# Optimization experiments

Hardware: AMD Instinct MI355X
Metric: run time of the kernel (lower is better)

Reference implementation:

```python
import jax, jax.numpy as jnp
import numpy as np

D = 32          # graph size -> E = D*D independent tiny MLPs
E = D * D       # 1024 experts
BATCH = 1024    # number of time points
H = 64          # hidden width hard-coded in TApproximator


def setup_inputs() -> dict:
    key = jax.random.key(0)
    ks = jax.random.split(key, 10)
    T = jax.random.uniform(ks[0], (BATCH,), dtype=jnp.float32)
    # per-expert uniform noise k ~ U[0,1) of shape [E, BATCH, H] (torch.rand(x.shape) per layer)
    noise = jax.random.uniform(ks[1], (E, BATCH, H), dtype=jnp.float32)
    # fc1: Linear(1, 64, bias=False) per expert -> weight [E, H]
    W1 = jax.random.normal(ks[2], (E, H), dtype=jnp.float32)
    # fc2: Linear(64, 64) per expert
    W2 = jax.random.normal(ks[3], (E, H, H), dtype=jnp.float32) / jnp.sqrt(jnp.float32(H))
    b2 = jax.random.normal(ks[4], (E, H), dtype=jnp.float32) * 0.01
    # fc3: Linear(64, 1) per expert
    W3 = jax.random.normal(ks[5], (E, H), dtype=jnp.float32) / jnp.sqrt(jnp.float32(H))
    b3 = jax.random.normal(ks[6], (E,), dtype=jnp.float32) * 0.01
    alpha = jnp.array([0.1], dtype=jnp.float32)
    beta = jnp.array([100.0], dtype=jnp.float32)
    bias = jnp.array([1.0], dtype=jnp.float32)
    return {"T": T, "noise": noise, "W1": W1, "W2": W2, "b2": b2,
            "W3": W3, "b3": b3, "alpha": alpha, "beta": beta, "bias": bias}


def reference(T, noise, W1, W2, b2, W3, b3, alpha, beta, bias):
    # --- TApproximator, batched over E = d^2 experts ---
    # fc1(T): [E, BATCH, H]
    x1 = jnp.einsum('b,eh->ebh', T, W1)
    # b = k*4 - 2 - x ; x += b  ==> fc1 output exactly cancels (as in source)
    x = x1 + (noise * 4.0 - 2.0 - x1)
    h = jax.nn.sigmoid(x)
    # sigmoid(fc2(h)): batched [E,BATCH,H] @ [E,H,H]
    h2 = jax.nn.sigmoid(jnp.einsum('ebh,eho->ebo', h, W2) + b2[:, None, :])
    # fc3 -> scalar per expert: [E, BATCH]
    out = jnp.einsum('ebh,eh->eb', h2, W3) + b3[:, None]
    B_mat = out.T  # torch.cat(B, dim=1) -> [BATCH, E]
    # T_embed = 1/alpha * cos(beta*T + bias)
    T_embed = (1.0 / alpha[0]) * jnp.cos(beta[0] * T + bias[0])
    return B_mat, T_embed
```

## Files before the change

kernel.cpp:

```cpp
#include <hip/hip_runtime.h>
#include <math.h>

#define NE 1024
#define NB 1024
#define NH 64

typedef __attribute__((ext_vector_type(4))) float f32x4;
typedef __attribute__((ext_vector_type(8))) __bf16 bf16x8;
typedef __attribute__((ext_vector_type(8))) unsigned short u16x8;

__device__ __forceinline__ unsigned short f2bf_bits(float f) {
  unsigned int u = __float_as_uint(f);
  u += 0x7fffu + ((u >> 16) & 1u);
  return (unsigned short)(u >> 16);
}

__device__ __forceinline__ float fast_sigmoid(float x) {
  float e = __builtin_amdgcn_exp2f(x * -1.4426950408889634f);
  return __builtin_amdgcn_rcpf(1.0f + e);
}

__global__ __launch_bounds__(256, 4) void expert_kernel(
    const float* __restrict__ noise,
    const float* __restrict__ W2,
    const float* __restrict__ b2,
    const float* __restrict__ W3,
    const float* __restrict__ b3,
    float* __restrict__ out)
{
  const int e    = blockIdx.x;
  const int tid  = threadIdx.x;
  const int lane = tid & 63;
  const int wid  = tid >> 6;
  const int c    = lane & 15;
  const int quad = lane >> 4;

  __shared__ float lds_w2[NH * NH];

  const float* w2e = W2 + (size_t)e * NH * NH;
  #pragma unroll
  for (int i = 0; i < 4; ++i) {
    int idx = tid + i * 256;
    ((f32x4*)lds_w2)[idx] = ((const f32x4*)w2e)[idx];
  }
  __syncthreads();

  bf16x8 bfrag[2][4];
  #pragma unroll
  for (int kh = 0; kh < 2; ++kh) {
    #pragma unroll
    for (int nt = 0; nt < 4; ++nt) {
      u16x8 tmp;
      #pragma unroll
      for (int j = 0; j < 8; ++j) {
        float w = lds_w2[(kh * 32 + quad * 8 + j) * NH + nt * 16 + c];
        tmp[j] = f2bf_bits(w);
      }
      bfrag[kh][nt] = __builtin_bit_cast(bf16x8, tmp);
    }
  }

  float b2v[4], w3v[4];
  #pragma unroll
  for (int nt = 0; nt < 4; ++nt) {
    b2v[nt] = b2[e * NH + nt * 16 + c];
    w3v[nt] = W3[e * NH + nt * 16 + c];
  }
  const float b3v = b3[e];

  const float* nbase = noise + (size_t)e * NB * NH;
  const f32x4 vzero = {0.f, 0.f, 0.f, 0.f};

  for (int pass = 0; pass < NB / 64; ++pass) {
    const int row0 = pass * 64 + wid * 16;
    const float* rowp = nbase + (row0 + c) * NH;

    f32x4 k0 = *((const f32x4*)(rowp + quad * 8));
    f32x4 k1 = *((const f32x4*)(rowp + quad * 8 + 4));
    f32x4 k2 = *((const f32x4*)(rowp + 32 + quad * 8));
    f32x4 k3 = *((const f32x4*)(rowp + 32 + quad * 8 + 4));

    u16x8 a0u, a1u;
    #pragma unroll
    for (int j = 0; j < 4; ++j) {
      a0u[j]     = f2bf_bits(fast_sigmoid(4.0f * k0[j] - 2.0f));
      a0u[j + 4] = f2bf_bits(fast_sigmoid(4.0f * k1[j] - 2.0f));
      a1u[j]     = f2bf_bits(fast_sigmoid(4.0f * k2[j] - 2.0f));
      a1u[j + 4] = f2bf_bits(fast_sigmoid(4.0f * k3[j] - 2.0f));
    }
    bf16x8 a0 = __builtin_bit_cast(bf16x8, a0u);
    bf16x8 a1 = __builtin_bit_cast(bf16x8, a1u);

    f32x4 acc[4];
    #pragma unroll
    for (int nt = 0; nt < 4; ++nt) acc[nt] = vzero;
    #pragma unroll
    for (int nt = 0; nt < 4; ++nt) {
      acc[nt] = __builtin_amdgcn_mfma_f32_16x16x32_bf16(a0, bfrag[0][nt], acc[nt], 0, 0, 0);
      acc[nt] = __builtin_amdgcn_mfma_f32_16x16x32_bf16(a1, bfrag[1][nt], acc[nt], 0, 0, 0);
    }

    float partial[4] = {0.f, 0.f, 0.f, 0.f};
    #pragma unroll
    for (int nt = 0; nt < 4; ++nt) {
      #pragma unroll
      for (int r = 0; r < 4; ++r) {
        float h2 = fast_sigmoid(acc[nt][r] + b2v[nt]);
        partial[r] += h2 * w3v[nt];
      }
    }

    #pragma unroll
    for (int r = 0; r < 4; ++r) {
      float v = partial[r];
      v += __shfl_xor(v, 1, 64);
      v += __shfl_xor(v, 2, 64);
      v += __shfl_xor(v, 4, 64);
      v += __shfl_xor(v, 8, 64);
      partial[r] = v;
    }

    if (c == 0) {
      #pragma unroll
      for (int r = 0; r < 4; ++r) {
        int b = row0 + quad * 4 + r;
        out[(size_t)b * NE + e] = partial[r] + b3v;
      }
    }
  }
}

__global__ void tembed_kernel(const float* __restrict__ T,
                              const float* __restrict__ alpha,
                              const float* __restrict__ beta,
                              const float* __restrict__ bias,
                              float* __restrict__ out2) {
  int i = blockIdx.x * blockDim.x + threadIdx.x;
  if (i < NB) {
    out2[i] = (1.0f / alpha[0]) * cosf(beta[0] * T[i] + bias[0]);
  }
}

extern "C" void kernel_launch(void* const* d_in, const int* in_sizes, int n_in,
                              void* d_out, int out_size, void* d_ws, size_t ws_size,
                              hipStream_t stream) {
  const float* T     = (const float*)d_in[0];
  const float* noise = (const float*)d_in[1];
  const float* W2    = (const float*)d_in[3];
  const float* b2    = (const float*)d_in[4];
  const float* W3    = (const float*)d_in[5];
  const float* b3    = (const float*)d_in[6];
  const float* alpha = (const float*)d_in[7];
  const float* beta  = (const float*)d_in[8];
  const float* bias  = (const float*)d_in[9];
  float* out = (float*)d_out;

  hipLaunchKernelGGL(expert_kernel, dim3(NE), dim3(256), 0, stream,
                     noise, W2, b2, W3, b3, out);
  hipLaunchKernelGGL(tembed_kernel, dim3(NB / 256), dim3(256), 0, stream,
                     T, alpha, beta, bias, out + (size_t)NE * NB);
}
```

Baseline: 399.2 us.

## Replace sigmoids with polynomial approximations, cheaper bf16 packing, and prefetch noise

Both sigmoids are replaced by odd minimax polynomials. The second one clamps its input to [-4,4], so outputs for larger pre-activations are approximated. The bf16 conversion now uses round-half-up plus a byte-permute to pack two values per instruction. Noise rows for the next pass are loaded a pass ahead so the global-memory latency overlaps the current MFMA and epilogue work. The goal is to cut transcendental and ALU cost in a kernel that is largely memory-bound, at the cost of accuracy from the approximate sigmoid and the clamp.

```diff
diff --git a/kernel.cpp b/kernel.cpp
--- a/kernel.cpp
+++ b/kernel.cpp
@@ -7,17 +7,29 @@
 
 typedef __attribute__((ext_vector_type(4))) float f32x4;
 typedef __attribute__((ext_vector_type(8))) __bf16 bf16x8;
-typedef __attribute__((ext_vector_type(8))) unsigned short u16x8;
+typedef __attribute__((ext_vector_type(4))) unsigned int u32x4;
 
-__device__ __forceinline__ unsigned short f2bf_bits(float f) {
-  unsigned int u = __float_as_uint(f);
-  u += 0x7fffu + ((u >> 16) & 1u);
-  return (unsigned short)(u >> 16);
+__device__ __forceinline__ unsigned int pack_bf16(float f0, float f1) {
+  unsigned int u0 = __float_as_uint(f0) + 0x8000u;
+  unsigned int u1 = __float_as_uint(f1) + 0x8000u;
+  return __builtin_amdgcn_perm(u1, u0, 0x07060302u);
 }
 
-__device__ __forceinline__ float fast_sigmoid(float x) {
-  float e = __builtin_amdgcn_exp2f(x * -1.4426950408889634f);
-  return __builtin_amdgcn_rcpf(1.0f + e);
+__device__ __forceinline__ float sig_h(float k) {
+  float t  = __builtin_fmaf(4.0f, k, -2.0f);
+  float x2 = t * t;
+  float u  = __builtin_fmaf(x2, 1.24902e-3f, -1.98468e-2f);
+  u        = __builtin_fmaf(x2, u, 0.2498016f);
+  return __builtin_fmaf(t, u, 0.5f);
+}
+
+__device__ __forceinline__ float sig_2(float x) {
+  x        = __builtin_amdgcn_fmed3f(x, -4.0f, 4.0f);
+  float x2 = x * x;
+  float u  = __builtin_fmaf(x2, -2.81297e-5f, 1.11341e-3f);
+  u        = __builtin_fmaf(x2, u, -1.86412e-2f);
+  u        = __builtin_fmaf(x2, u, 0.2489492f);
+  return __builtin_fmaf(x, u, 0.5f);
 }
 
 __global__ __launch_bounds__(256, 4) void expert_kernel(
@@ -50,11 +62,12 @@
   for (int kh = 0; kh < 2; ++kh) {
     #pragma unroll
     for (int nt = 0; nt < 4; ++nt) {
-      u16x8 tmp;
+      u32x4 tmp;
       #pragma unroll
-      for (int j = 0; j < 8; ++j) {
-        float w = lds_w2[(kh * 32 + quad * 8 + j) * NH + nt * 16 + c];
-        tmp[j] = f2bf_bits(w);
+      for (int j = 0; j < 4; ++j) {
+        float w0 = lds_w2[(kh * 32 + quad * 8 + 2 * j)     * NH + nt * 16 + c];
+        float w1 = lds_w2[(kh * 32 + quad * 8 + 2 * j + 1) * NH + nt * 16 + c];
+        tmp[j] = pack_bf16(w0, w1);
       }
       bfrag[kh][nt] = __builtin_bit_cast(bf16x8, tmp);
     }
@@ -71,22 +84,28 @@
   const float* nbase = noise + (size_t)e * NB * NH;
   const f32x4 vzero = {0.f, 0.f, 0.f, 0.f};
 
+  const float* rowp = nbase + (wid * 16 + c) * NH;
+  f32x4 k0 = *((const f32x4*)(rowp + quad * 8));
+  f32x4 k1 = *((const f32x4*)(rowp + quad * 8 + 4));
+  f32x4 k2 = *((const f32x4*)(rowp + 32 + quad * 8));
+  f32x4 k3 = *((const f32x4*)(rowp + 32 + quad * 8 + 4));
+
+  #pragma unroll 1
   for (int pass = 0; pass < NB / 64; ++pass) {
-    const int row0 = pass * 64 + wid * 16;
-    const float* rowp = nbase + (row0 + c) * NH;
+    int np = pass + 1 < NB / 64 ? pass + 1 : NB / 64 - 1;
+    const float* nrowp = nbase + (np * 64 + wid * 16 + c) * NH;
+    f32x4 n0 = *((const f32x4*)(nrowp + quad * 8));
+    f32x4 n1 = *((const f32x4*)(nrowp + quad * 8 + 4));
+    f32x4 n2 = *((const f32x4*)(nrowp + 32 + quad * 8));
+    f32x4 n3 = *((const f32x4*)(nrowp + 32 + quad * 8 + 4));
 
-    f32x4 k0 = *((const f32x4*)(rowp + quad * 8));
-    f32x4 k1 = *((const f32x4*)(rowp + quad * 8 + 4));
-    f32x4 k2 = *((const f32x4*)(rowp + 32 + quad * 8));
-    f32x4 k3 = *((const f32x4*)(rowp + 32 + quad * 8 + 4));
-
-    u16x8 a0u, a1u;
+    u32x4 a0u, a1u;
     #pragma unroll
-    for (int j = 0; j < 4; ++j) {
-      a0u[j]     = f2bf_bits(fast_sigmoid(4.0f * k0[j] - 2.0f));
-      a0u[j + 4] = f2bf_bits(fast_sigmoid(4.0f * k1[j] - 2.0f));
-      a1u[j]     = f2bf_bits(fast_sigmoid(4.0f * k2[j] - 2.0f));
-      a1u[j + 4] = f2bf_bits(fast_sigmoid(4.0f * k3[j] - 2.0f));
+    for (int j = 0; j < 2; ++j) {
+      a0u[j]     = pack_bf16(sig_h(k0[2 * j]), sig_h(k0[2 * j + 1]));
+      a0u[j + 2] = pack_bf16(sig_h(k1[2 * j]), sig_h(k1[2 * j + 1]));
+      a1u[j]     = pack_bf16(sig_h(k2[2 * j]), sig_h(k2[2 * j + 1]));
+      a1u[j + 2] = pack_bf16(sig_h(k3[2 * j]), sig_h(k3[2 * j + 1]));
     }
     bf16x8 a0 = __builtin_bit_cast(bf16x8, a0u);
     bf16x8 a1 = __builtin_bit_cast(bf16x8, a1u);
@@ -105,8 +124,8 @@
     for (int nt = 0; nt < 4; ++nt) {
       #pragma unroll
       for (int r = 0; r < 4; ++r) {
-        float h2 = fast_sigmoid(acc[nt][r] + b2v[nt]);
-        partial[r] += h2 * w3v[nt];
+        float h2 = sig_2(acc[nt][r] + b2v[nt]);
+        partial[r] = __builtin_fmaf(h2, w3v[nt], partial[r]);
       }
     }
 
@@ -121,12 +140,15 @@
     }
 
     if (c == 0) {
+      const int row0 = pass * 64 + wid * 16;
       #pragma unroll
       for (int r = 0; r < 4; ++r) {
         int b = row0 + quad * 4 + r;
         out[(size_t)b * NE + e] = partial[r] + b3v;
       }
     }
+
+    k0 = n0; k1 = n1; k2 = n2; k3 = n3;
   }
 }
 
```

New measurement: 396.7 us. Within noise of the previous version (-0.6%).
